# Kernel tuning notes

Hardware: AMD Instinct MI355X
Metric: run time of the kernel (lower is better)

## Reference

```python
import jax, jax.numpy as jnp
import numpy as np

B, S, E, H, V, T = 64, 64, 256, 512, 50000, 32
SOS, PAD = 1, 0


def setup_inputs() -> dict:
    key = jax.random.key(0)
    ks = jax.random.split(key, 12)
    sc = 0.05
    embedding = jax.random.normal(ks[0], (V, E), jnp.float32) * sc
    embedding = embedding.at[PAD].set(0.0)  # padding_idx row is zero
    inp = {
        "encoder_hidden": jax.random.normal(ks[1], (1, B, H), jnp.float32),
        "target": jax.random.randint(ks[2], (B, T), 0, V),
        "target_length": jax.random.randint(ks[3], (B,), 1, T + 1),
        "encoder_outputs": jax.random.normal(ks[4], (B, S, H), jnp.float32),
        "embedding": embedding,
        "w_ih": jax.random.normal(ks[5], (3 * H, E), jnp.float32) * sc,
        "w_hh": jax.random.normal(ks[6], (3 * H, H), jnp.float32) * sc,
        "b_ih": jnp.zeros((3 * H,), jnp.float32),
        "b_hh": jnp.zeros((3 * H,), jnp.float32),
        "attn_w": jax.random.normal(ks[7], (H, H), jnp.float32) * sc,  # Attention 'general' W
        "Wa": jax.random.normal(ks[8], (H, 2 * H), jnp.float32) * sc,  # concat projection (no bias)
        "fc_w": jax.random.normal(ks[9], (V, H), jnp.float32) * sc,
        "fc_b": jnp.zeros((V,), jnp.float32),
    }
    return inp


def _gru_cell(x, h, w_ih, w_hh, b_ih, b_hh):
    # PyTorch GRU cell math. x: [B,E], h: [B,H]
    gi = x @ w_ih.T + b_ih          # [B,3H]
    gh = h @ w_hh.T + b_hh          # [B,3H]
    i_r, i_z, i_n = jnp.split(gi, 3, axis=-1)
    h_r, h_z, h_n = jnp.split(gh, 3, axis=-1)
    r = jax.nn.sigmoid(i_r + h_r)
    z = jax.nn.sigmoid(i_z + h_z)
    n = jnp.tanh(i_n + r * h_n)
    return (1.0 - z) * n + z * h


def reference(encoder_hidden, target, target_length, encoder_outputs, embedding,
              w_ih, w_hh, b_ih, b_hh, attn_w, Wa, fc_w, fc_b):
    h0 = encoder_hidden[0]                                   # [B,H]
    # Luong 'general' attention: precompute W_attn @ encoder_outputs once
    enc_proj = jnp.einsum("bsh,gh->bsg", encoder_outputs, attn_w)  # [B,S,H]
    init_input = jnp.full((B,), SOS, dtype=jnp.int32)

    def step(carry, _):
        dec_in, h = carry
        x = embedding[dec_in]                                # [B,E]
        h_new = _gru_cell(x, h, w_ih, w_hh, b_ih, b_hh)      # [B,H]
        scores = jnp.einsum("bh,bsh->bs", h_new, enc_proj)   # [B,S]
        attn_weights = jax.nn.softmax(scores, axis=-1)
        context = jnp.einsum("bs,bsh->bh", attn_weights, encoder_outputs)
        concat = jnp.concatenate([h_new, context], axis=-1)  # [B,2H]
        concat_out = jnp.tanh(concat @ Wa.T)                 # [B,H]
        logits = jax.nn.log_softmax(concat_out @ fc_w.T + fc_b, axis=-1)  # [B,V]
        nxt = jnp.argmax(logits, axis=-1).astype(jnp.int32)  # topk(1) -> greedy
        return (nxt, h_new), logits

    (_, h_fin), outs = jax.lax.scan(step, (init_input, h0), None, length=T)
    decoder_outputs = jnp.transpose(outs, (1, 0, 2))          # [B,T,V]
    return decoder_outputs, h_fin[None]                       # ([B,T,V], [1,B,H])
```

## Files before the change

### kernel.cpp

```cpp
#include <hip/hip_runtime.h>
#include <hip/hip_bf16.h>
#include <math.h>

#define B_ 64
#define S_ 64
#define E_ 256
#define H_ 512
#define V_ 50000
#define T_ 32
#define SOS_ 1
#define NCHUNK 196
#define MARGIN 0.25f
static const long long LDCV = (long long)T_ * V_;

typedef unsigned short u16;
typedef unsigned long long u64;
typedef u16   u16x8  __attribute__((ext_vector_type(8)));
typedef short bf16x8 __attribute__((ext_vector_type(8)));
typedef float f32x4  __attribute__((ext_vector_type(4)));

static __device__ __forceinline__ u16 f2bf(float f) {
    unsigned u = __float_as_uint(f);
    unsigned r = (u + 0x7FFFu + ((u >> 16) & 1u)) >> 16;
    return (u16)r;
}
static __device__ __forceinline__ unsigned pk2(float a, float b) {
    __hip_bfloat162 t = __float22bfloat162_rn(make_float2(a, b));
    unsigned r; __builtin_memcpy(&r, &t, 4); return r;
}
static __device__ __forceinline__ unsigned fenc(float f) {
    unsigned u = __float_as_uint(f);
    return u ^ ((u & 0x80000000u) ? 0xFFFFFFFFu : 0x80000000u);
}
static __device__ __forceinline__ float fdec(unsigned e) {
    unsigned u = (e & 0x80000000u) ? (e ^ 0x80000000u) : ~e;
    return __uint_as_float(u);
}

__global__ __launch_bounds__(256) void build_wbig(
    const float* __restrict__ w_ih, const float* __restrict__ w_hh,
    const float* __restrict__ b_ih, const float* __restrict__ b_hh,
    float* __restrict__ WbigT, float* __restrict__ biasBig)
{
    for (int g = blockIdx.x * 256 + threadIdx.x; g < 2048 * 768;
         g += gridDim.x * 256) {
        int n = g / 768, k = g % 768;
        int j = n >> 2, c = n & 3;
        float v = 0.f;
        if (c == 0)      v = (k < 256) ? w_ih[j * 256 + k]          : w_hh[j * 512 + (k - 256)];
        else if (c == 1) v = (k < 256) ? w_ih[(512 + j) * 256 + k]  : w_hh[(512 + j) * 512 + (k - 256)];
        else if (c == 2) v = (k < 256) ? w_ih[(1024 + j) * 256 + k] : 0.f;
        else             v = (k < 256) ? 0.f                        : w_hh[(1024 + j) * 512 + (k - 256)];
        WbigT[g] = v;
    }
    int g0 = blockIdx.x * 256 + threadIdx.x;
    if (g0 < 2048) {
        int j = g0 >> 2, c = g0 & 3;
        float bv;
        if (c == 0)      bv = b_ih[j] + b_hh[j];
        else if (c == 1) bv = b_ih[512 + j] + b_hh[512 + j];
        else if (c == 2) bv = b_ih[1024 + j];
        else             bv = b_hh[1024 + j];
        biasBig[g0] = bv;
    }
}

__global__ __launch_bounds__(256) void transpose_aw(
    const float* __restrict__ attn_w, float* __restrict__ awT)
{
    int idx = blockIdx.x * 256 + threadIdx.x;
    int h = idx >> 9, g = idx & 511;
    awT[idx] = attn_w[g * 512 + h];
}

__global__ __launch_bounds__(256) void init_state(
    const float* __restrict__ enc_hidden, float* __restrict__ hbuf0,
    u64* __restrict__ win64, unsigned* __restrict__ rowmax)
{
    int idx = blockIdx.x * 256 + threadIdx.x;
    if (idx < B_ * H_) hbuf0[idx] = enc_hidden[idx];
    if (idx < B_) {
        win64[idx] = (u64)(~(unsigned)SOS_);
        rowmax[idx] = 0u;
    }
}

__global__ __launch_bounds__(256) void conv_fcw(
    const float* __restrict__ fc_w, u16* __restrict__ fcwb)
{
    const size_t total = (size_t)V_ * 512;
    const size_t stride = (size_t)gridDim.x * 256 * 8;
    for (size_t i = ((size_t)blockIdx.x * 256 + threadIdx.x) * 8; i < total;
         i += stride) {
        float4 a = *(const float4*)&fc_w[i];
        float4 b = *(const float4*)&fc_w[i + 4];
        u16x8 o;
        o[0] = f2bf(a.x); o[1] = f2bf(a.y); o[2] = f2bf(a.z); o[3] = f2bf(a.w);
        o[4] = f2bf(b.x); o[5] = f2bf(b.y); o[6] = f2bf(b.z); o[7] = f2bf(b.w);
        *(u16x8*)&fcwb[i] = o;
    }
}

__global__ __launch_bounds__(256) void gruh(
    const float* __restrict__ WbigT, const float* __restrict__ biasBig,
    const float* __restrict__ emb, const u64* __restrict__ win64,
    const float* __restrict__ hcur, float* __restrict__ hnxt,
    float* __restrict__ concatA)
{
    __shared__ float As[64][36];
    __shared__ float Ws[64][36];
    const int tid = threadIdx.x;
    const int nb = blockIdx.x & 63;
    const int mb = blockIdx.x >> 6;
    const int n0 = nb * 32, m0 = mb * 32;
    const int tm = tid & 31;
    const int tn = tid >> 5;
    float acc[4] = {0.f, 0.f, 0.f, 0.f};
    int tokm[2];
    #pragma unroll
    for (int r = 0; r < 2; ++r) {
        int m = (tid + r * 256) >> 4;
        tokm[r] = (int)(~(unsigned)(win64[m0 + m] & 0xFFFFFFFFull));
    }

    for (int k0 = 0; k0 < 768; k0 += 64) {
        #pragma unroll
        for (int r = 0; r < 2; ++r) {
            int idx = tid + r * 256;
            int m = idx >> 4;
            int kk = (idx & 15) << 2;
            int k = k0 + kk;
            float4 v = (k < 256)
                ? *(const float4*)&emb[(size_t)tokm[r] * 256 + k]
                : *(const float4*)&hcur[(m0 + m) * 512 + (k - 256)];
            As[kk + 0][m] = v.x; As[kk + 1][m] = v.y;
            As[kk + 2][m] = v.z; As[kk + 3][m] = v.w;
        }
        #pragma unroll
        for (int r = 0; r < 2; ++r) {
            int idx = tid + r * 256;
            int n = idx >> 4;
            int kk = (idx & 15) << 2;
            float4 v = *(const float4*)&WbigT[(size_t)(n0 + n) * 768 + k0 + kk];
            Ws[kk + 0][n] = v.x; Ws[kk + 1][n] = v.y;
            Ws[kk + 2][n] = v.z; Ws[kk + 3][n] = v.w;
        }
        __syncthreads();
        #pragma unroll
        for (int kk = 0; kk < 64; ++kk) {
            float a = As[kk][tm];
            float4 w = *(const float4*)&Ws[kk][tn << 2];
            acc[0] += a * w.x; acc[1] += a * w.y;
            acc[2] += a * w.z; acc[3] += a * w.w;
        }
        __syncthreads();
    }

    int jg = (n0 >> 2) + tn;
    float b0 = biasBig[(jg << 2) + 0], b1 = biasBig[(jg << 2) + 1];
    float b2 = biasBig[(jg << 2) + 2], b3 = biasBig[(jg << 2) + 3];
    int m = m0 + tm;
    float g0 = acc[0] + b0, g1 = acc[1] + b1;
    float g2 = acc[2] + b2, g3 = acc[3] + b3;
    float r_ = 1.f / (1.f + expf(-g0));
    float z_ = 1.f / (1.f + expf(-g1));
    float nn = tanhf(g2 + r_ * g3);
    float hv = hcur[m * 512 + jg];
    float h2 = (1.f - z_) * nn + z_ * hv;
    hnxt[m * 512 + jg] = h2;
    concatA[m * 1024 + jg] = h2;
}

__global__ __launch_bounds__(256) void attnq(
    const float* __restrict__ hnew, const float* __restrict__ awT,
    const float* __restrict__ enc, float* __restrict__ concatA)
{
    int b = blockIdx.x, tid = threadIdx.x;
    __shared__ float hs[512], q[512], aw[64];
    hs[tid] = hnew[b * 512 + tid];
    hs[tid + 256] = hnew[b * 512 + 256 + tid];
    __syncthreads();
    #pragma unroll
    for (int hh = 0; hh < 2; ++hh) {
        int h = tid + hh * 256;
        const float4* wr = (const float4*)(awT + (size_t)h * 512);
        float a = 0.f;
        #pragma unroll 8
        for (int k = 0; k < 128; ++k) {
            float4 w4 = wr[k];
            a += hs[4 * k] * w4.x + hs[4 * k + 1] * w4.y
               + hs[4 * k + 2] * w4.z + hs[4 * k + 3] * w4.w;
        }
        q[h] = a;
    }
    __syncthreads();
    int wv = tid >> 6, ln = tid & 63;
    for (int si = 0; si < 16; ++si) {
        int s = wv * 16 + si;
        const float* er = enc + ((size_t)(b * 64 + s)) * 512;
        float p = 0.f;
        #pragma unroll
        for (int i = 0; i < 8; ++i) p += q[ln + (i << 6)] * er[ln + (i << 6)];
        for (int off = 32; off; off >>= 1) p += __shfl_down(p, off);
        if (ln == 0) aw[s] = p;
    }
    __syncthreads();
    if (tid < 64) {
        float v = aw[tid], m = v;
        for (int off = 32; off; off >>= 1) m = fmaxf(m, __shfl_xor(m, off));
        float e = __expf(v - m);
        float ssum = e;
        for (int off = 32; off; off >>= 1) ssum += __shfl_xor(ssum, off);
        aw[tid] = e / ssum;
    }
    __syncthreads();
    #pragma unroll
    for (int hh = 0; hh < 2; ++hh) {
        int h = tid + hh * 256;
        float c = 0.f;
        const float* eb = enc + (size_t)b * 64 * 512 + h;
        #pragma unroll 8
        for (int s = 0; s < 64; ++s) c += aw[s] * eb[s * 512];
        concatA[b * 1024 + 512 + h] = c;
    }
}

__global__ __launch_bounds__(256) void ctxtanh(
    const float* __restrict__ concatA, const float* __restrict__ Wa,
    float* __restrict__ Abuf, u16* __restrict__ Abufb,
    u64* __restrict__ win64, unsigned* __restrict__ rowmax)
{
    __shared__ float As[64][20];
    __shared__ float Ws[64][20];
    const int tid = threadIdx.x;
    const int nb = blockIdx.x & 31;
    const int mb = blockIdx.x >> 5;
    const int n0 = nb * 16, m0 = mb * 16;
    const int tm = tid & 15, tn = tid >> 4;
    if (blockIdx.x == 0 && tid < 64) {
        win64[tid] = 0ull;
        rowmax[tid] = 0u;
    }
    float acc = 0.f;

    for (int k0 = 0; k0 < 1024; k0 += 64) {
        {
            int m = tid >> 4;
            int kk = (tid & 15) << 2;
            float4 v = *(const float4*)&concatA[(size_t)(m0 + m) * 1024 + k0 + kk];
            As[kk + 0][m] = v.x; As[kk + 1][m] = v.y;
            As[kk + 2][m] = v.z; As[kk + 3][m] = v.w;
        }
        {
            int n = tid >> 4;
            int kk = (tid & 15) << 2;
            float4 v = *(const float4*)&Wa[(size_t)(n0 + n) * 1024 + k0 + kk];
            Ws[kk + 0][n] = v.x; Ws[kk + 1][n] = v.y;
            Ws[kk + 2][n] = v.z; Ws[kk + 3][n] = v.w;
        }
        __syncthreads();
        #pragma unroll
        for (int kk = 0; kk < 64; ++kk)
            acc += As[kk][tm] * Ws[kk][tn];
        __syncthreads();
    }
    float th = tanhf(acc);
    int m = m0 + tm, n = n0 + tn;
    Abuf[m * 512 + n] = th;
    Abufb[m * 512 + n] = f2bf(th);
}

template <int CACHED>
__global__ __launch_bounds__(256) void logits_mfma(
    const u16* __restrict__ Abufb, const float* __restrict__ fcw,
    const u16* __restrict__ fcwb, const float* __restrict__ fc_b,
    float* __restrict__ outp, float* __restrict__ pmax,
    float* __restrict__ psum, unsigned* __restrict__ rowmax)
{
    __shared__ u16 sA[64 * 512];
    const int tid = threadIdx.x;
    const int wv = tid >> 6, lane = tid & 63;
    const int nb = blockIdx.x * 256;
    const int col16 = lane & 15, grp = lane >> 4;

    #pragma unroll
    for (int i = 0; i < 16; ++i) {
        int c = tid + i * 256;
        int m = c >> 6;
        int cb = (c & 63) << 4;
        int sb = cb ^ ((m & 7) << 4);
        *(u16x8*)((char*)sA + m * 1024 + sb) =
            *(const u16x8*)(Abufb + m * 512 + (cb >> 1));
    }
    __syncthreads();

    int nfb[4]; bool val[4];
    #pragma unroll
    for (int fn = 0; fn < 4; ++fn) {
        nfb[fn] = nb + wv * 64 + fn * 16;
        val[fn] = nfb[fn] < V_;
    }

    f32x4 acc[4][4];
    #pragma unroll
    for (int a = 0; a < 4; ++a)
        #pragma unroll
        for (int b2 = 0; b2 < 4; ++b2) acc[a][b2] = (f32x4){0.f, 0.f, 0.f, 0.f};

    if (CACHED) {
        const u16* wpb[4];
        #pragma unroll
        for (int fn = 0; fn < 4; ++fn) {
            size_t rowi = val[fn] ? (size_t)(nfb[fn] + col16) : 0;
            wpb[fn] = fcwb + rowi * 512 + (grp << 3);
        }
        bf16x8 bcur[4];
        #pragma unroll
        for (int fn = 0; fn < 4; ++fn) bcur[fn] = *(const bf16x8*)(wpb[fn]);
        for (int kt = 0; kt < 16; ++kt) {
            bf16x8 bnxt[4];
            int ktn = (kt < 15) ? kt + 1 : 15;
            #pragma unroll
            for (int fn = 0; fn < 4; ++fn)
                bnxt[fn] = *(const bf16x8*)(wpb[fn] + ktn * 32);
            bf16x8 af[4];
            int kb = kt * 64 + (grp << 4);
            #pragma unroll
            for (int fm = 0; fm < 4; ++fm) {
                int mg = fm * 16 + col16;
                af[fm] = *(const bf16x8*)((const char*)sA + mg * 1024 + (kb ^ ((mg & 7) << 4)));
            }
            #pragma unroll
            for (int fm = 0; fm < 4; ++fm)
                #pragma unroll
                for (int fn = 0; fn < 4; ++fn)
                    acc[fm][fn] = __builtin_amdgcn_mfma_f32_16x16x32_bf16(
                        af[fm], bcur[fn], acc[fm][fn], 0, 0, 0);
            #pragma unroll
            for (int fn = 0; fn < 4; ++fn) bcur[fn] = bnxt[fn];
        }
    } else {
        const float* wp[4];
        #pragma unroll
        for (int fn = 0; fn < 4; ++fn) {
            size_t rowi = val[fn] ? (size_t)(nfb[fn] + col16) : 0;
            wp[fn] = fcw + rowi * 512 + (grp << 3);
        }
        float4 lo[4], hi[4];
        #pragma unroll
        for (int fn = 0; fn < 4; ++fn) {
            lo[fn] = *(const float4*)(wp[fn]);
            hi[fn] = *(const float4*)(wp[fn] + 4);
        }
        for (int kt = 0; kt < 16; ++kt) {
            float4 nl[4], nh[4];
            int ktn = (kt < 15) ? kt + 1 : 15;
            #pragma unroll
            for (int fn = 0; fn < 4; ++fn) {
                nl[fn] = *(const float4*)(wp[fn] + ktn * 32);
                nh[fn] = *(const float4*)(wp[fn] + ktn * 32 + 4);
            }
            bf16x8 bc[4];
            #pragma unroll
            for (int fn = 0; fn < 4; ++fn) {
                union { unsigned u[4]; bf16x8 v; } cv;
                cv.u[0] = pk2(lo[fn].x, lo[fn].y);
                cv.u[1] = pk2(lo[fn].z, lo[fn].w);
                cv.u[2] = pk2(hi[fn].x, hi[fn].y);
                cv.u[3] = pk2(hi[fn].z, hi[fn].w);
                bc[fn] = cv.v;
            }
            bf16x8 af[4];
            int kb = kt * 64 + (grp << 4);
            #pragma unroll
            for (int fm = 0; fm < 4; ++fm) {
                int mg = fm * 16 + col16;
                af[fm] = *(const bf16x8*)((const char*)sA + mg * 1024 + (kb ^ ((mg & 7) << 4)));
            }
            #pragma unroll
            for (int fm = 0; fm < 4; ++fm)
                #pragma unroll
                for (int fn = 0; fn < 4; ++fn)
                    acc[fm][fn] = __builtin_amdgcn_mfma_f32_16x16x32_bf16(
                        af[fm], bc[fn], acc[fm][fn], 0, 0, 0);
            #pragma unroll
            for (int fn = 0; fn < 4; ++fn) { lo[fn] = nl[fn]; hi[fn] = nh[fn]; }
        }
    }
    __syncthreads();

    float* wmaxp = (float*)sA;
    float* wsump = (float*)(sA + 512);

    float bias[4];
    #pragma unroll
    for (int fn = 0; fn < 4; ++fn) bias[fn] = val[fn] ? fc_b[nfb[fn] + col16] : 0.f;

    #pragma unroll
    for (int fm = 0; fm < 4; ++fm) {
        #pragma unroll
        for (int r = 0; r < 4; ++r) {
            int mrow = fm * 16 + grp * 4 + r;
            float best = -INFINITY;
            float vv[4];
            #pragma unroll
            for (int fn = 0; fn < 4; ++fn) {
                float v = -INFINITY;
                if (val[fn]) {
                    v = acc[fm][fn][r] + bias[fn];
                    outp[(size_t)mrow * LDCV + nfb[fn] + col16] = v;
                    best = fmaxf(best, v);
                }
                vv[fn] = v;
            }
            #pragma unroll
            for (int d = 1; d < 16; d <<= 1) best = fmaxf(best, __shfl_xor(best, d));
            float s = 0.f;
            #pragma unroll
            for (int fn = 0; fn < 4; ++fn)
                if (val[fn]) s += __expf(vv[fn] - best);
            #pragma unroll
            for (int d = 1; d < 16; d <<= 1) s += __shfl_xor(s, d);
            if (col16 == 0) {
                wmaxp[wv * 64 + mrow] = best;
                wsump[wv * 64 + mrow] = s;
            }
        }
    }
    __syncthreads();
    if (tid < 64) {
        float gm = -INFINITY;
        #pragma unroll
        for (int w = 0; w < 4; ++w) gm = fmaxf(gm, wmaxp[w * 64 + tid]);
        float gs = 0.f;
        #pragma unroll
        for (int w = 0; w < 4; ++w)
            gs += wsump[w * 64 + tid] * __expf(wmaxp[w * 64 + tid] - gm);
        pmax[tid * NCHUNK + blockIdx.x] = gm;
        psum[tid * NCHUNK + blockIdx.x] = gs;
        atomicMax(rowmax + tid, fenc(gm));
    }
}

__global__ __launch_bounds__(256) void candrefine(
    const float* __restrict__ pmax, const float* __restrict__ psum,
    const float* __restrict__ out, const float* __restrict__ Abuf,
    const float* __restrict__ fcw, const float* __restrict__ fc_b,
    const unsigned* __restrict__ rowmax, u64* __restrict__ win64,
    float* __restrict__ logZ_arr, int t)
{
    const int c = blockIdx.x, b = blockIdx.y, tid = threadIdx.x;
    __shared__ float sv[256];

    float Mb = fdec(rowmax[b]);

    if (c == 0) {
        float pm_ = (tid < NCHUNK) ? pmax[b * NCHUNK + tid] : -INFINITY;
        sv[tid] = (tid < NCHUNK) ? psum[b * NCHUNK + tid] * __expf(pm_ - Mb) : 0.f;
        __syncthreads();
        for (int st = 128; st; st >>= 1) {
            if (tid < st) sv[tid] += sv[tid + st];
            __syncthreads();
        }
        if (tid == 0) logZ_arr[b * T_ + t] = Mb + logf(sv[0]);
        __syncthreads();
    }

    if (pmax[b * NCHUNK + c] < Mb - MARGIN) return;

    __shared__ float A[512];
    __shared__ u64 sp[256];
    A[tid] = Abuf[b * 512 + tid];
    A[tid + 256] = Abuf[b * 512 + 256 + tid];
    __syncthreads();

    u64 pk = 0ull;
    int n = c * 256 + tid;
    if (n < V_) {
        float L = out[(size_t)b * LDCV + (size_t)t * V_ + n];
        if (L >= Mb - MARGIN) {
            const float* wr = fcw + (size_t)n * 512;
            float d = fc_b[n];
            #pragma unroll 8
            for (int k = 0; k < 512; k += 4) {
                float4 w4 = *(const float4*)&wr[k];
                d += A[k] * w4.x + A[k + 1] * w4.y + A[k + 2] * w4.z + A[k + 3] * w4.w;
            }
            pk = ((u64)fenc(d) << 32) | (u64)(~(unsigned)n);
        }
    }
    sp[tid] = pk;
    __syncthreads();
    for (int st = 128; st; st >>= 1) {
        if (tid < st) { u64 o = sp[tid + st]; if (o > sp[tid]) sp[tid] = o; }
        __syncthreads();
    }
    if (tid == 0 && sp[0] != 0ull) atomicMax(&win64[b], sp[0]);
}

__global__ __launch_bounds__(256) void norm_all(
    float* __restrict__ out, const float* __restrict__ logZ_arr)
{
    int row = blockIdx.x;
    float z = logZ_arr[row];
    float4* base = (float4*)(out + (size_t)row * V_);
    for (int j = threadIdx.x; j < 12500; j += 256) {
        float4 v = base[j];
        v.x -= z; v.y -= z; v.z -= z; v.w -= z;
        base[j] = v;
    }
}

__global__ __launch_bounds__(256) void final_copy(
    const float* __restrict__ hfin, float* __restrict__ dst)
{
    int idx = blockIdx.x * 256 + threadIdx.x;
    if (idx < B_ * H_) dst[idx] = hfin[idx];
}

extern "C" void kernel_launch(void* const* d_in, const int* in_sizes, int n_in,
                              void* d_out, int out_size, void* d_ws, size_t ws_size,
                              hipStream_t stream)
{
    const float* enc_hidden = (const float*)d_in[0];
    const float* enc    = (const float*)d_in[3];
    const float* emb    = (const float*)d_in[4];
    const float* w_ih   = (const float*)d_in[5];
    const float* w_hh   = (const float*)d_in[6];
    const float* b_ih   = (const float*)d_in[7];
    const float* b_hh   = (const float*)d_in[8];
    const float* attn_w = (const float*)d_in[9];
    const float* Wa     = (const float*)d_in[10];
    const float* fc_w   = (const float*)d_in[11];
    const float* fc_b   = (const float*)d_in[12];
    float* out = (float*)d_out;
    float* ws  = (float*)d_ws;

    size_t off = 0;
    float* WbigT   = ws + off; off += 1572864;
    float* biasBig = ws + off; off += 2048;
    float* awT     = ws + off; off += 262144;
    float* hbuf0   = ws + off; off += 32768;
    float* hbuf1   = ws + off; off += 32768;
    float* concatA = ws + off; off += 65536;
    float* Abuf    = ws + off; off += 32768;
    u16*   Abufb   = (u16*)(ws + off); off += 16384;
    float* pmax    = ws + off; off += 64 * NCHUNK;
    float* psum    = ws + off; off += 64 * NCHUNK;
    float* logZ_a  = ws + off; off += 64 * T_;
    unsigned* rowmax = (unsigned*)(ws + off); off += 64;
    off = (off + 1) & ~(size_t)1;
    u64*   win64   = (u64*)(ws + off); off += 128;
    off = (off + 3) & ~(size_t)3;
    u16*   fcwb    = (u16*)(ws + off);
    const bool big = ws_size >= (off + 12800000) * 4;

    build_wbig<<<1536, 256, 0, stream>>>(w_ih, w_hh, b_ih, b_hh, WbigT, biasBig);
    transpose_aw<<<1024, 256, 0, stream>>>(attn_w, awT);
    init_state<<<128, 256, 0, stream>>>(enc_hidden, hbuf0, win64, rowmax);
    if (big) conv_fcw<<<2048, 256, 0, stream>>>(fc_w, fcwb);

    for (int t = 0; t < T_; ++t) {
        float* hcur = (t & 1) ? hbuf1 : hbuf0;
        float* hnxt = (t & 1) ? hbuf0 : hbuf1;
        float* outp = out + (size_t)t * V_;

        gruh<<<128, 256, 0, stream>>>(WbigT, biasBig, emb, win64, hcur, hnxt, concatA);
        attnq<<<64, 256, 0, stream>>>(hnxt, awT, enc, concatA);
        ctxtanh<<<128, 256, 0, stream>>>(concatA, Wa, Abuf, Abufb, win64, rowmax);
        if (big)
            logits_mfma<1><<<NCHUNK, 256, 0, stream>>>(
                Abufb, fc_w, fcwb, fc_b, outp, pmax, psum, rowmax);
        else
            logits_mfma<0><<<NCHUNK, 256, 0, stream>>>(
                Abufb, fc_w, fcwb, fc_b, outp, pmax, psum, rowmax);
        candrefine<<<dim3(NCHUNK, B_), 256, 0, stream>>>(
            pmax, psum, out, Abuf, fc_w, fc_b, rowmax, win64, logZ_a, t);
    }

    norm_all<<<2048, 256, 0, stream>>>(out, logZ_a);
    final_copy<<<128, 256, 0, stream>>>(hbuf0, out + (size_t)B_ * T_ * V_);
}
```

Before: 5.168 ms.

## Fuse attention with concat projection and defer logZ computation after decode loop

Merges the attention kernel and the concat-projection/tanh kernel into one per-batch-row kernel that keeps the concatenated vector in shared memory, so the concatA buffer and one launch per step go away. The log-partition reduction moves out of candrefine into a single logz_kernel after the loop, working on per-step pmax/psum arrays saved for every step. This cuts launches and serial work on the per-step critical path. The cost is more workspace, and the Wa projection now runs on only 64 blocks with no tiling, reading the Wa weight once per block.

```diff
diff --git a/kernel.cpp b/kernel.cpp
--- a/kernel.cpp
+++ b/kernel.cpp
@@ -104,8 +104,7 @@
 __global__ __launch_bounds__(256) void gruh(
     const float* __restrict__ WbigT, const float* __restrict__ biasBig,
     const float* __restrict__ emb, const u64* __restrict__ win64,
-    const float* __restrict__ hcur, float* __restrict__ hnxt,
-    float* __restrict__ concatA)
+    const float* __restrict__ hcur, float* __restrict__ hnxt)
 {
     __shared__ float As[64][36];
     __shared__ float Ws[64][36];
@@ -168,17 +167,20 @@
     float hv = hcur[m * 512 + jg];
     float h2 = (1.f - z_) * nn + z_ * hv;
     hnxt[m * 512 + jg] = h2;
-    concatA[m * 1024 + jg] = h2;
-}
-
-__global__ __launch_bounds__(256) void attnq(
+}
+
+__global__ __launch_bounds__(256) void attnctx(
     const float* __restrict__ hnew, const float* __restrict__ awT,
-    const float* __restrict__ enc, float* __restrict__ concatA)
+    const float* __restrict__ enc, const float* __restrict__ Wa,
+    float* __restrict__ Abuf, u16* __restrict__ Abufb,
+    u64* __restrict__ win64, unsigned* __restrict__ rowmax)
 {
     int b = blockIdx.x, tid = threadIdx.x;
-    __shared__ float hs[512], q[512], aw[64];
-    hs[tid] = hnew[b * 512 + tid];
-    hs[tid + 256] = hnew[b * 512 + 256 + tid];
+    __shared__ float cc[1024];
+    __shared__ float q[512], aw[64];
+    if (tid == 0) { win64[b] = 0ull; rowmax[b] = 0u; }
+    cc[tid] = hnew[b * 512 + tid];
+    cc[tid + 256] = hnew[b * 512 + 256 + tid];
     __syncthreads();
     #pragma unroll
     for (int hh = 0; hh < 2; ++hh) {
@@ -188,8 +190,8 @@
         #pragma unroll 8
         for (int k = 0; k < 128; ++k) {
             float4 w4 = wr[k];
-            a += hs[4 * k] * w4.x + hs[4 * k + 1] * w4.y
-               + hs[4 * k + 2] * w4.z + hs[4 * k + 3] * w4.w;
+            a += cc[4 * k] * w4.x + cc[4 * k + 1] * w4.y
+               + cc[4 * k + 2] * w4.z + cc[4 * k + 3] * w4.w;
         }
         q[h] = a;
     }
@@ -221,53 +223,26 @@
         const float* eb = enc + (size_t)b * 64 * 512 + h;
         #pragma unroll 8
         for (int s = 0; s < 64; ++s) c += aw[s] * eb[s * 512];
-        concatA[b * 1024 + 512 + h] = c;
-    }
-}
-
-__global__ __launch_bounds__(256) void ctxtanh(
-    const float* __restrict__ concatA, const float* __restrict__ Wa,
-    float* __restrict__ Abuf, u16* __restrict__ Abufb,
-    u64* __restrict__ win64, unsigned* __restrict__ rowmax)
-{
-    __shared__ float As[64][20];
-    __shared__ float Ws[64][20];
-    const int tid = threadIdx.x;
-    const int nb = blockIdx.x & 31;
-    const int mb = blockIdx.x >> 5;
-    const int n0 = nb * 16, m0 = mb * 16;
-    const int tm = tid & 15, tn = tid >> 4;
-    if (blockIdx.x == 0 && tid < 64) {
-        win64[tid] = 0ull;
-        rowmax[tid] = 0u;
-    }
-    float acc = 0.f;
-
-    for (int k0 = 0; k0 < 1024; k0 += 64) {
-        {
-            int m = tid >> 4;
-            int kk = (tid & 15) << 2;
-            float4 v = *(const float4*)&concatA[(size_t)(m0 + m) * 1024 + k0 + kk];
-            As[kk + 0][m] = v.x; As[kk + 1][m] = v.y;
-            As[kk + 2][m] = v.z; As[kk + 3][m] = v.w;
-        }
-        {
-            int n = tid >> 4;
-            int kk = (tid & 15) << 2;
-            float4 v = *(const float4*)&Wa[(size_t)(n0 + n) * 1024 + k0 + kk];
-            Ws[kk + 0][n] = v.x; Ws[kk + 1][n] = v.y;
-            Ws[kk + 2][n] = v.z; Ws[kk + 3][n] = v.w;
-        }
-        __syncthreads();
-        #pragma unroll
-        for (int kk = 0; kk < 64; ++kk)
-            acc += As[kk][tm] * Ws[kk][tn];
-        __syncthreads();
-    }
-    float th = tanhf(acc);
-    int m = m0 + tm, n = n0 + tn;
-    Abuf[m * 512 + n] = th;
-    Abufb[m * 512 + n] = f2bf(th);
+        cc[512 + h] = c;
+    }
+    __syncthreads();
+    #pragma unroll
+    for (int hh = 0; hh < 2; ++hh) {
+        int n = tid + hh * 256;
+        const float* wr = Wa + (size_t)n * 1024;
+        float acc = 0.f;
+        #pragma unroll 4
+        for (int k = 0; k < 1024; k += 4) {
+            float4 w4 = *(const float4*)&wr[k];
+            acc += cc[k] * w4.x;
+            acc += cc[k + 1] * w4.y;
+            acc += cc[k + 2] * w4.z;
+            acc += cc[k + 3] * w4.w;
+        }
+        float th = tanhf(acc);
+        Abuf[b * 512 + n] = th;
+        Abufb[b * 512 + n] = f2bf(th);
+    }
 }
 
 template <int CACHED>
@@ -443,29 +418,13 @@
 }
 
 __global__ __launch_bounds__(256) void candrefine(
-    const float* __restrict__ pmax, const float* __restrict__ psum,
-    const float* __restrict__ out, const float* __restrict__ Abuf,
-    const float* __restrict__ fcw, const float* __restrict__ fc_b,
-    const unsigned* __restrict__ rowmax, u64* __restrict__ win64,
-    float* __restrict__ logZ_arr, int t)
+    const float* __restrict__ pmax, const float* __restrict__ outp,
+    const float* __restrict__ Abuf, const float* __restrict__ fcw,
+    const float* __restrict__ fc_b, const unsigned* __restrict__ rowmax,
+    u64* __restrict__ win64)
 {
     const int c = blockIdx.x, b = blockIdx.y, tid = threadIdx.x;
-    __shared__ float sv[256];
-
     float Mb = fdec(rowmax[b]);
-
-    if (c == 0) {
-        float pm_ = (tid < NCHUNK) ? pmax[b * NCHUNK + tid] : -INFINITY;
-        sv[tid] = (tid < NCHUNK) ? psum[b * NCHUNK + tid] * __expf(pm_ - Mb) : 0.f;
-        __syncthreads();
-        for (int st = 128; st; st >>= 1) {
-            if (tid < st) sv[tid] += sv[tid + st];
-            __syncthreads();
-        }
-        if (tid == 0) logZ_arr[b * T_ + t] = Mb + logf(sv[0]);
-        __syncthreads();
-    }
-
     if (pmax[b * NCHUNK + c] < Mb - MARGIN) return;
 
     __shared__ float A[512];
@@ -477,7 +436,7 @@
     u64 pk = 0ull;
     int n = c * 256 + tid;
     if (n < V_) {
-        float L = out[(size_t)b * LDCV + (size_t)t * V_ + n];
+        float L = outp[(size_t)b * LDCV + n];
         if (L >= Mb - MARGIN) {
             const float* wr = fcw + (size_t)n * 512;
             float d = fc_b[n];
@@ -496,6 +455,24 @@
         __syncthreads();
     }
     if (tid == 0 && sp[0] != 0ull) atomicMax(&win64[b], sp[0]);
+}
+
+__global__ __launch_bounds__(256) void logz_kernel(
+    const float* __restrict__ pmaxT, const float* __restrict__ psumT,
+    float* __restrict__ logZ_arr)
+{
+    int t = blockIdx.x, b = blockIdx.y, tid = threadIdx.x;
+    __shared__ float sv[256];
+    const float* pm = pmaxT + ((size_t)t * 64 + b) * NCHUNK;
+    const float* ps = psumT + ((size_t)t * 64 + b) * NCHUNK;
+    float p = (tid < NCHUNK) ? pm[tid] : -INFINITY;
+    sv[tid] = p; __syncthreads();
+    for (int st = 128; st; st >>= 1) { if (tid < st) sv[tid] = fmaxf(sv[tid], sv[tid + st]); __syncthreads(); }
+    float Mb = sv[0]; __syncthreads();
+    sv[tid] = (tid < NCHUNK) ? ps[tid] * __expf(p - Mb) : 0.f;
+    __syncthreads();
+    for (int st = 128; st; st >>= 1) { if (tid < st) sv[tid] += sv[tid + st]; __syncthreads(); }
+    if (tid == 0) logZ_arr[b * T_ + t] = Mb + logf(sv[0]);
 }
 
 __global__ __launch_bounds__(256) void norm_all(
@@ -542,11 +519,10 @@
     float* awT     = ws + off; off += 262144;
     float* hbuf0   = ws + off; off += 32768;
     float* hbuf1   = ws + off; off += 32768;
-    float* concatA = ws + off; off += 65536;
     float* Abuf    = ws + off; off += 32768;
     u16*   Abufb   = (u16*)(ws + off); off += 16384;
-    float* pmax    = ws + off; off += 64 * NCHUNK;
-    float* psum    = ws + off; off += 64 * NCHUNK;
+    float* pmaxT   = ws + off; off += (size_t)T_ * 64 * NCHUNK;
+    float* psumT   = ws + off; off += (size_t)T_ * 64 * NCHUNK;
     float* logZ_a  = ws + off; off += 64 * T_;
     unsigned* rowmax = (unsigned*)(ws + off); off += 64;
     off = (off + 1) & ~(size_t)1;
@@ -564,20 +540,22 @@
         float* hcur = (t & 1) ? hbuf1 : hbuf0;
         float* hnxt = (t & 1) ? hbuf0 : hbuf1;
         float* outp = out + (size_t)t * V_;
-
-        gruh<<<128, 256, 0, stream>>>(WbigT, biasBig, emb, win64, hcur, hnxt, concatA);
-        attnq<<<64, 256, 0, stream>>>(hnxt, awT, enc, concatA);
-        ctxtanh<<<128, 256, 0, stream>>>(concatA, Wa, Abuf, Abufb, win64, rowmax);
+        float* pmS = pmaxT + (size_t)t * 64 * NCHUNK;
+        float* psS = psumT + (size_t)t * 64 * NCHUNK;
+
+        gruh<<<128, 256, 0, stream>>>(WbigT, biasBig, emb, win64, hcur, hnxt);
+        attnctx<<<64, 256, 0, stream>>>(hnxt, awT, enc, Wa, Abuf, Abufb, win64, rowmax);
         if (big)
             logits_mfma<1><<<NCHUNK, 256, 0, stream>>>(
-                Abufb, fc_w, fcwb, fc_b, outp, pmax, psum, rowmax);
+                Abufb, fc_w, fcwb, fc_b, outp, pmS, psS, rowmax);
         else
             logits_mfma<0><<<NCHUNK, 256, 0, stream>>>(
-                Abufb, fc_w, fcwb, fc_b, outp, pmax, psum, rowmax);
+                Abufb, fc_w, fcwb, fc_b, outp, pmS, psS, rowmax);
         candrefine<<<dim3(NCHUNK, B_), 256, 0, stream>>>(
-            pmax, psum, out, Abuf, fc_w, fc_b, rowmax, win64, logZ_a, t);
-    }
-
+            pmS, outp, Abuf, fc_w, fc_b, rowmax, win64);
+    }
+
+    logz_kernel<<<dim3(T_, B_), 256, 0, stream>>>(pmaxT, psumT, logZ_a);
     norm_all<<<2048, 256, 0, stream>>>(out, logZ_a);
     final_copy<<<128, 256, 0, stream>>>(hbuf0, out + (size_t)B_ * T_ * V_);
 }
```

Result: slower. 6.071 ms (+17.5%).

## Defer logZ reduction out of decode loop and coarsen candidate refine blocks

Applied to the files above, without the earlier changes.

Per-step partial max/sum arrays are now stored per timestep so the log-sum-exp normalizer is computed once after the loop in a new logz kernel, removing that reduction from the serial per-step critical path. The candidate refinement kernel now handles four chunks per block (49 blocks per row instead of 196), cutting the number of early-exit blocks launched each step. The cost is extra workspace for the per-step partials and a serialized loop over chunks inside each surviving block. The logZ kernel recomputes the row max from the partial maxima rather than reading rowmax.

```diff
diff --git a/kernel.cpp b/kernel.cpp
--- a/kernel.cpp
+++ b/kernel.cpp
@@ -443,30 +443,18 @@
 }
 
 __global__ __launch_bounds__(256) void candrefine(
-    const float* __restrict__ pmax, const float* __restrict__ psum,
-    const float* __restrict__ out, const float* __restrict__ Abuf,
-    const float* __restrict__ fcw, const float* __restrict__ fc_b,
-    const unsigned* __restrict__ rowmax, u64* __restrict__ win64,
-    float* __restrict__ logZ_arr, int t)
-{
-    const int c = blockIdx.x, b = blockIdx.y, tid = threadIdx.x;
-    __shared__ float sv[256];
-
+    const float* __restrict__ pmax, const float* __restrict__ outp,
+    const float* __restrict__ Abuf, const float* __restrict__ fcw,
+    const float* __restrict__ fc_b, const unsigned* __restrict__ rowmax,
+    u64* __restrict__ win64)
+{
+    const int b = blockIdx.y, tid = threadIdx.x;
+    const int c0 = blockIdx.x * 4;
     float Mb = fdec(rowmax[b]);
-
-    if (c == 0) {
-        float pm_ = (tid < NCHUNK) ? pmax[b * NCHUNK + tid] : -INFINITY;
-        sv[tid] = (tid < NCHUNK) ? psum[b * NCHUNK + tid] * __expf(pm_ - Mb) : 0.f;
-        __syncthreads();
-        for (int st = 128; st; st >>= 1) {
-            if (tid < st) sv[tid] += sv[tid + st];
-            __syncthreads();
-        }
-        if (tid == 0) logZ_arr[b * T_ + t] = Mb + logf(sv[0]);
-        __syncthreads();
-    }
-
-    if (pmax[b * NCHUNK + c] < Mb - MARGIN) return;
+    float4 pm4 = *(const float4*)&pmax[b * NCHUNK + c0];
+    float thr = Mb - MARGIN;
+    if (!(pm4.x >= thr || pm4.y >= thr || pm4.z >= thr || pm4.w >= thr))
+        return;
 
     __shared__ float A[512];
     __shared__ u64 sp[256];
@@ -474,28 +462,53 @@
     A[tid + 256] = Abuf[b * 512 + 256 + tid];
     __syncthreads();
 
-    u64 pk = 0ull;
-    int n = c * 256 + tid;
-    if (n < V_) {
-        float L = out[(size_t)b * LDCV + (size_t)t * V_ + n];
-        if (L >= Mb - MARGIN) {
-            const float* wr = fcw + (size_t)n * 512;
-            float d = fc_b[n];
-            #pragma unroll 8
-            for (int k = 0; k < 512; k += 4) {
-                float4 w4 = *(const float4*)&wr[k];
-                d += A[k] * w4.x + A[k + 1] * w4.y + A[k + 2] * w4.z + A[k + 3] * w4.w;
-            }
-            pk = ((u64)fenc(d) << 32) | (u64)(~(unsigned)n);
-        }
-    }
-    sp[tid] = pk;
-    __syncthreads();
-    for (int st = 128; st; st >>= 1) {
-        if (tid < st) { u64 o = sp[tid + st]; if (o > sp[tid]) sp[tid] = o; }
+    float pmv[4] = {pm4.x, pm4.y, pm4.z, pm4.w};
+    #pragma unroll
+    for (int i = 0; i < 4; ++i) {
+        if (pmv[i] < thr) continue;
+        int n = (c0 + i) * 256 + tid;
+        u64 pk = 0ull;
+        if (n < V_) {
+            float L = outp[(size_t)b * LDCV + n];
+            if (L >= thr) {
+                const float* wr = fcw + (size_t)n * 512;
+                float d = fc_b[n];
+                #pragma unroll 8
+                for (int k = 0; k < 512; k += 4) {
+                    float4 w4 = *(const float4*)&wr[k];
+                    d += A[k] * w4.x + A[k + 1] * w4.y
+                       + A[k + 2] * w4.z + A[k + 3] * w4.w;
+                }
+                pk = ((u64)fenc(d) << 32) | (u64)(~(unsigned)n);
+            }
+        }
+        sp[tid] = pk;
         __syncthreads();
-    }
-    if (tid == 0 && sp[0] != 0ull) atomicMax(&win64[b], sp[0]);
+        for (int st = 128; st; st >>= 1) {
+            if (tid < st) { u64 o = sp[tid + st]; if (o > sp[tid]) sp[tid] = o; }
+            __syncthreads();
+        }
+        if (tid == 0 && sp[0] != 0ull) atomicMax(&win64[b], sp[0]);
+        __syncthreads();
+    }
+}
+
+__global__ __launch_bounds__(256) void logz_kernel(
+    const float* __restrict__ pmaxT, const float* __restrict__ psumT,
+    float* __restrict__ logZ_arr)
+{
+    int t = blockIdx.x, b = blockIdx.y, tid = threadIdx.x;
+    __shared__ float sv[256];
+    const float* pm = pmaxT + ((size_t)t * 64 + b) * NCHUNK;
+    const float* ps = psumT + ((size_t)t * 64 + b) * NCHUNK;
+    float p = (tid < NCHUNK) ? pm[tid] : -INFINITY;
+    sv[tid] = p; __syncthreads();
+    for (int st = 128; st; st >>= 1) { if (tid < st) sv[tid] = fmaxf(sv[tid], sv[tid + st]); __syncthreads(); }
+    float Mb = sv[0]; __syncthreads();
+    sv[tid] = (tid < NCHUNK) ? ps[tid] * __expf(p - Mb) : 0.f;
+    __syncthreads();
+    for (int st = 128; st; st >>= 1) { if (tid < st) sv[tid] += sv[tid + st]; __syncthreads(); }
+    if (tid == 0) logZ_arr[b * T_ + t] = Mb + logf(sv[0]);
 }
 
 __global__ __launch_bounds__(256) void norm_all(
@@ -545,8 +558,8 @@
     float* concatA = ws + off; off += 65536;
     float* Abuf    = ws + off; off += 32768;
     u16*   Abufb   = (u16*)(ws + off); off += 16384;
-    float* pmax    = ws + off; off += 64 * NCHUNK;
-    float* psum    = ws + off; off += 64 * NCHUNK;
+    float* pmaxT   = ws + off; off += (size_t)T_ * 64 * NCHUNK;
+    float* psumT   = ws + off; off += (size_t)T_ * 64 * NCHUNK;
     float* logZ_a  = ws + off; off += 64 * T_;
     unsigned* rowmax = (unsigned*)(ws + off); off += 64;
     off = (off + 1) & ~(size_t)1;
@@ -564,20 +577,23 @@
         float* hcur = (t & 1) ? hbuf1 : hbuf0;
         float* hnxt = (t & 1) ? hbuf0 : hbuf1;
         float* outp = out + (size_t)t * V_;
+        float* pmS = pmaxT + (size_t)t * 64 * NCHUNK;
+        float* psS = psumT + (size_t)t * 64 * NCHUNK;
 
         gruh<<<128, 256, 0, stream>>>(WbigT, biasBig, emb, win64, hcur, hnxt, concatA);
         attnq<<<64, 256, 0, stream>>>(hnxt, awT, enc, concatA);
         ctxtanh<<<128, 256, 0, stream>>>(concatA, Wa, Abuf, Abufb, win64, rowmax);
         if (big)
             logits_mfma<1><<<NCHUNK, 256, 0, stream>>>(
-                Abufb, fc_w, fcwb, fc_b, outp, pmax, psum, rowmax);
+                Abufb, fc_w, fcwb, fc_b, outp, pmS, psS, rowmax);
         else
             logits_mfma<0><<<NCHUNK, 256, 0, stream>>>(
-                Abufb, fc_w, fcwb, fc_b, outp, pmax, psum, rowmax);
-        candrefine<<<dim3(NCHUNK, B_), 256, 0, stream>>>(
-            pmax, psum, out, Abuf, fc_w, fc_b, rowmax, win64, logZ_a, t);
-    }
-
+                Abufb, fc_w, fcwb, fc_b, outp, pmS, psS, rowmax);
+        candrefine<<<dim3(49, B_), 256, 0, stream>>>(
+            pmS, outp, Abuf, fc_w, fc_b, rowmax, win64);
+    }
+
+    logz_kernel<<<dim3(T_, B_), 256, 0, stream>>>(pmaxT, psumT, logZ_a);
     norm_all<<<2048, 256, 0, stream>>>(out, logZ_a);
     final_copy<<<128, 256, 0, stream>>>(hbuf0, out + (size_t)B_ * T_ * V_);
 }
```

After: 5.584 ms. 8.1% more time.
